# Optimization experiments

Measured on AMD Instinct MI355X. Metric: run time of the kernel, lower is better.

## Reference

```python
import jax, jax.numpy as jnp
import numpy as np

RATIOS = [0.9, 0.7, 0.5, 0.3]
EPS = 1e-5


def _layernorm(x, g, b):
    m = jnp.mean(x, axis=-1, keepdims=True)
    v = jnp.mean(jnp.square(x - m), axis=-1, keepdims=True)
    return (x - m) * jax.lax.rsqrt(v + EPS) * g + b


def _stage(x, g, b, W, bias):
    return _layernorm(x, g, b) @ W + bias


def _prune(x, W1, b1, W2, b2, ratio):
    B, N, C = x.shape
    stats = jnp.mean(x, axis=1)                       # (B, C)
    scores = jax.nn.relu(stats @ W1 + b1) @ W2 + b2    # (B, C)
    k = max(1, int(C * ratio))
    _, idx = jax.lax.top_k(jax.lax.stop_gradient(scores), k)  # (B, k)
    hard = jnp.zeros((B, C), scores.dtype).at[jnp.arange(B)[:, None], idx].set(1.0)
    soft = jax.nn.sigmoid(scores)
    # straight-through: forward value == hard, gradient flows through soft
    mask = hard + soft - jax.lax.stop_gradient(soft)
    return x * mask[:, None, :]


def setup_inputs() -> dict:
    key = jax.random.key(0)
    dims = [(96, 96), (96, 192), (192, 384), (384, 768)]
    inp = {}
    ks = jax.random.split(key, 64)
    ki = iter(ks)
    inp["x"] = jax.random.normal(next(ki), (32, 3136, 96), dtype=jnp.float32)
    for i, (din, dout) in enumerate(dims, 1):
        inp[f"s{i}_g"] = jnp.ones((din,), jnp.float32)
        inp[f"s{i}_b"] = jnp.zeros((din,), jnp.float32)
        inp[f"s{i}_W"] = jax.random.normal(next(ki), (din, dout), jnp.float32) * 0.02
        inp[f"s{i}_bias"] = jnp.zeros((dout,), jnp.float32)
        d = dout
        inp[f"p{i}_W1"] = jax.random.normal(next(ki), (d, d // 4), jnp.float32) * 0.02
        inp[f"p{i}_b1"] = jnp.zeros((d // 4,), jnp.float32)
        inp[f"p{i}_W2"] = jax.random.normal(next(ki), (d // 4, d), jnp.float32) * 0.02
        inp[f"p{i}_b2"] = jnp.zeros((d,), jnp.float32)
    inp["H"] = 56
    inp["W"] = 56
    return inp


def reference(x,
              s1_g, s1_b, s1_W, s1_bias, p1_W1, p1_b1, p1_W2, p1_b2,
              s2_g, s2_b, s2_W, s2_bias, p2_W1, p2_b1, p2_W2, p2_b2,
              s3_g, s3_b, s3_W, s3_bias, p3_W1, p3_b1, p3_W2, p3_b2,
              s4_g, s4_b, s4_W, s4_bias, p4_W1, p4_b1, p4_W2, p4_b2,
              H, W):
    x = _stage(x, s1_g, s1_b, s1_W, s1_bias)
    x = _prune(x, p1_W1, p1_b1, p1_W2, p1_b2, RATIOS[0])
    x = _stage(x, s2_g, s2_b, s2_W, s2_bias)
    x = _prune(x, p2_W1, p2_b1, p2_W2, p2_b2, RATIOS[1])
    x = _stage(x, s3_g, s3_b, s3_W, s3_bias)
    x = _prune(x, p3_W1, p3_b1, p3_W2, p3_b2, RATIOS[2])
    x = _stage(x, s4_g, s4_b, s4_W, s4_bias)
    x = _prune(x, p4_W1, p4_b1, p4_W2, p4_b2, RATIOS[3])
    return x
```

## Files before the change

kernel.cpp:

```cpp
#include <hip/hip_runtime.h>
#include <hip/hip_bf16.h>
#include <stdint.h>

#define NTOK 3136
#define MTOT 100352
#define RPW  14
#define WPB  224

typedef __attribute__((ext_vector_type(8))) short bf16x8;
typedef __attribute__((ext_vector_type(4))) float f32x4;
typedef __attribute__((ext_vector_type(2))) float f32x2;

static __device__ __forceinline__ ushort f2bf(float x) {
  union { float f; uint32_t u; } c; c.f = x;
  uint32_t r = (c.u + 0x7FFFu + ((c.u >> 16) & 1u)) >> 16;
  return (ushort)r;
}
static __device__ __forceinline__ float bf2f(ushort h) {
  union { uint32_t u; float f; } c; c.u = ((uint32_t)h) << 16;
  return c.f;
}

template<int DIN, bool WLO>
__global__ __launch_bounds__(256)
void ln_colsum_k(const float* __restrict__ in, const float* __restrict__ gma,
                 const float* __restrict__ bta, ushort* __restrict__ oh,
                 ushort* __restrict__ ol, float* __restrict__ part)
{
  constexpr int P2 = DIN / 2;
  constexpr int T2 = (P2 + 63) / 64;
  const int wid  = (blockIdx.x * 256 + threadIdx.x) >> 6;
  const int lane = threadIdx.x & 63;
  const int b = wid / WPB;
  const int w = wid - b * WPB;

  f32x2 gv[T2], bv[T2], acc[T2];
#pragma unroll
  for (int t = 0; t < T2; ++t) {
    int c2 = lane + 64 * t;
    if (c2 < P2) {
      gv[t] = *(const f32x2*)(gma + 2 * c2);
      bv[t] = *(const f32x2*)(bta + 2 * c2);
    } else { gv[t] = {0.f, 0.f}; bv[t] = {0.f, 0.f}; }
    acc[t] = {0.f, 0.f};
  }

  const size_t rbase = ((size_t)b * NTOK + (size_t)w * RPW) * DIN;
  const float* ip = in + rbase;
  ushort* oph = oh + rbase;
  ushort* opl = ol + rbase;

  for (int j = 0; j < RPW; ++j) {
    f32x2 v[T2];
    float s = 0.f, sq = 0.f;
#pragma unroll
    for (int t = 0; t < T2; ++t) {
      int c2 = lane + 64 * t;
      f32x2 xv = {0.f, 0.f};
      if (c2 < P2) xv = *(const f32x2*)(ip + (size_t)j * DIN + 2 * c2);
      v[t] = xv;
      s  += xv[0] + xv[1];
      sq += xv[0] * xv[0] + xv[1] * xv[1];
    }
#pragma unroll
    for (int off = 1; off < 64; off <<= 1) {
      s  += __shfl_xor(s, off);
      sq += __shfl_xor(sq, off);
    }
    float m   = s / (float)DIN;
    float var = sq / (float)DIN - m * m;
    float r   = 1.f / sqrtf(var + 1e-5f);
#pragma unroll
    for (int t = 0; t < T2; ++t) {
      int c2 = lane + 64 * t;
      if (c2 < P2) {
        float xn0 = (v[t][0] - m) * r * gv[t][0] + bv[t][0];
        float xn1 = (v[t][1] - m) * r * gv[t][1] + bv[t][1];
        ushort h0 = f2bf(xn0), h1 = f2bf(xn1);
        ((uint32_t*)(oph + (size_t)j * DIN))[c2] =
            (uint32_t)h0 | ((uint32_t)h1 << 16);
        if (WLO) {
          ushort l0 = f2bf(xn0 - bf2f(h0)), l1 = f2bf(xn1 - bf2f(h1));
          ((uint32_t*)(opl + (size_t)j * DIN))[c2] =
              (uint32_t)l0 | ((uint32_t)l1 << 16);
        }
        acc[t][0] += xn0;
        acc[t][1] += xn1;
      }
    }
  }
#pragma unroll
  for (int t = 0; t < T2; ++t) {
    int c2 = lane + 64 * t;
    if (c2 < P2) {
      int c = 2 * c2;
      part[((size_t)b * DIN + c) * WPB + w]     = acc[t][0];
      part[((size_t)b * DIN + c + 1) * WPB + w] = acc[t][1];
    }
  }
}

template<int DIN, int DOUT, int SLOTS, bool CMP, int CMPN, int RLEN, bool GLO>
__global__ __launch_bounds__(1024)
void scores_k(const float* __restrict__ part,
              const float* __restrict__ Wt, const float* __restrict__ bias,
              const float* __restrict__ W1, const float* __restrict__ b1,
              const float* __restrict__ W2, const float* __restrict__ b2,
              float* __restrict__ mask, int k,
              const ushort* __restrict__ whi, const ushort* __restrict__ wlo,
              ushort* __restrict__ wch, ushort* __restrict__ wcl,
              int* __restrict__ list_g, float* __restrict__ biasc)
{
  constexpr int DH  = DOUT / 4;
  constexpr int DH4 = DH / 4;
  constexpr int NSLC = (1024 / DH4 < 64) ? 1024 / DH4 : 64;
  constexpr int RPSC = (DOUT + NSLC - 1) / NSLC;
  constexpr int C4  = DOUT / 4;
  constexpr int NSLD = (1024 / C4 < 64) ? 1024 / C4 : 64;
  constexpr int RPSD = (DH + NSLD - 1) / NSLD;

  __shared__ float xm[DIN];
  __shared__ float st[DOUT];
  __shared__ float h[DH];
  __shared__ float sc[DOUT];
  __shared__ float red[4096];
  __shared__ int lsh[256];

  const int b = blockIdx.x, tid = threadIdx.x;

  if constexpr (SLOTS == 25) {
    if (tid < DIN) {
      const float* p = part + ((size_t)b * DIN + tid) * 25;
      float s = 0.f;
#pragma unroll
      for (int i = 0; i < 25; ++i) s += p[i];
      xm[tid] = s * (1.f / (float)NTOK);
    }
  } else {
    const int cg = tid >> 2, wq = tid & 3;
    if (cg < DIN) {
      const float* p = part + ((size_t)b * DIN + cg) * WPB + wq * 56;
      f32x4 a = {0.f, 0.f, 0.f, 0.f};
#pragma unroll
      for (int u = 0; u < 14; ++u) {
        f32x4 t0 = *(const f32x4*)(p + u * 4);
        a[0] += t0[0]; a[1] += t0[1]; a[2] += t0[2]; a[3] += t0[3];
      }
      red[wq * DIN + cg] = (a[0] + a[1]) + (a[2] + a[3]);
    }
    __syncthreads();
    if (tid < DIN)
      xm[tid] = ((red[0 * DIN + tid] + red[1 * DIN + tid]) +
                 (red[2 * DIN + tid] + red[3 * DIN + tid])) * (1.f / (float)NTOK);
  }
  __syncthreads();

  {
    constexpr int RPS = DIN / 4;
    const int j4 = tid % C4, sl = tid / C4;
    if (sl < 4) {
      const float* wp = Wt + (size_t)(sl * RPS) * DOUT + j4 * 4;
      f32x4 acc = {0.f, 0.f, 0.f, 0.f};
#pragma unroll
      for (int r = 0; r < RPS; ++r) {
        f32x4 wv = *(const f32x4*)(wp + (size_t)r * DOUT);
        float xv = xm[sl * RPS + r];
        acc[0] = fmaf(xv, wv[0], acc[0]);
        acc[1] = fmaf(xv, wv[1], acc[1]);
        acc[2] = fmaf(xv, wv[2], acc[2]);
        acc[3] = fmaf(xv, wv[3], acc[3]);
      }
      *(f32x4*)&red[sl * DOUT + j4 * 4] = acc;
    }
  }
  __syncthreads();
  if (tid < DOUT)
    st[tid] = ((red[0 * DOUT + tid] + red[1 * DOUT + tid]) +
               (red[2 * DOUT + tid] + red[3 * DOUT + tid])) + bias[tid];
  __syncthreads();

  {
    const int j4 = tid % DH4, sl = tid / DH4;
    if (sl < NSLC) {
      f32x4 acc = {0.f, 0.f, 0.f, 0.f};
#pragma unroll
      for (int rr = 0; rr < RPSC; ++rr) {
        int r = sl * RPSC + rr;
        if (r < DOUT) {
          f32x4 wv = *(const f32x4*)(W1 + (size_t)r * DH + j4 * 4);
          float sv = st[r];
          acc[0] = fmaf(sv, wv[0], acc[0]);
          acc[1] = fmaf(sv, wv[1], acc[1]);
          acc[2] = fmaf(sv, wv[2], acc[2]);
          acc[3] = fmaf(sv, wv[3], acc[3]);
        }
      }
      *(f32x4*)&red[(size_t)sl * DH + j4 * 4] = acc;
    }
  }
  __syncthreads();
  if (tid < DH) {
    float a = 0.f;
#pragma unroll 4
    for (int sl = 0; sl < NSLC; ++sl) a += red[(size_t)sl * DH + tid];
    h[tid] = fmaxf(b1[tid] + a, 0.f);
  }
  __syncthreads();

  {
    const int c4 = tid % C4, sl = tid / C4;
    if (sl < NSLD) {
      f32x4 acc = {0.f, 0.f, 0.f, 0.f};
#pragma unroll
      for (int rr = 0; rr < RPSD; ++rr) {
        int r = sl * RPSD + rr;
        if (r < DH) {
          f32x4 wv = *(const f32x4*)(W2 + (size_t)r * DOUT + c4 * 4);
          float hv = h[r];
          acc[0] = fmaf(hv, wv[0], acc[0]);
          acc[1] = fmaf(hv, wv[1], acc[1]);
          acc[2] = fmaf(hv, wv[2], acc[2]);
          acc[3] = fmaf(hv, wv[3], acc[3]);
        }
      }
      *(f32x4*)&red[(size_t)sl * DOUT + c4 * 4] = acc;
    }
  }
  __syncthreads();
  for (int c = tid; c < DOUT; c += 1024) {
    float a = 0.f;
#pragma unroll 4
    for (int sl = 0; sl < NSLD; ++sl) a += red[(size_t)sl * DOUT + c];
    sc[c] = b2[c] + a;
  }
  __syncthreads();

  for (int c = tid; c < DOUT; c += 1024) {
    float v = sc[c];
    int rank = 0;
#pragma unroll 8
    for (int j = 0; j < DOUT; ++j) {
      float u = sc[j];
      rank += (u > v) || (u == v && j < c);
    }
    mask[(size_t)b * DOUT + c] = (rank < k) ? 1.f : 0.f;
    if (CMP && rank < k) lsh[rank] = c;
  }
  if constexpr (CMP) {
    if (tid >= k && tid < CMPN) lsh[tid] = -1;
    __syncthreads();
    if (tid < CMPN) {
      int c = lsh[tid];
      list_g[b * 256 + tid] = c;
      biasc[b * 256 + tid] = (c >= 0) ? bias[c] : 0.f;
    }
    constexpr int U4 = RLEN / 8;
    for (int idx = tid; idx < CMPN * U4; idx += 1024) {
      int j = idx / U4, u = idx - j * U4;
      int src = lsh[j];
      uint4 v = make_uint4(0u, 0u, 0u, 0u);
      if (src >= 0) v = *(const uint4*)(whi + (size_t)src * RLEN + u * 8);
      *(uint4*)(wch + ((size_t)b * CMPN + j) * RLEN + u * 8) = v;
      if constexpr (GLO) {
        uint4 vl = make_uint4(0u, 0u, 0u, 0u);
        if (src >= 0) vl = *(const uint4*)(wlo + (size_t)src * RLEN + u * 8);
        *(uint4*)(wcl + ((size_t)b * CMPN + j) * RLEN + u * 8) = vl;
      }
    }
  }
}

__global__ __launch_bounds__(256)
void convW_all_k(const float* __restrict__ W0, const float* __restrict__ W1,
                 const float* __restrict__ W2, const float* __restrict__ W3,
                 ushort* __restrict__ hi, ushort* __restrict__ lo)
{
  const int Kd[4]   = { 96, 96, 192, 384 };
  const int Nd[4]   = { 96, 192, 384, 768 };
  const int off[5]  = { 0, 12288, 36864, 110592, 405504 };
  const float* Wp[4] = { W0, W1, W2, W3 };

  int idx = blockIdx.x * 256 + threadIdx.x;
  if (idx >= 405504) return;
  int s = (idx >= off[1]) + (idx >= off[2]) + (idx >= off[3]);
  int local = idx - off[s];
  int K = Kd[s], N = Nd[s];
  int n = local / K, kk = local - n * K;
  float v = (n < N) ? Wp[s][(size_t)kk * N + n] : 0.f;
  ushort h = f2bf(v);
  hi[idx] = h;
  lo[idx] = f2bf(v - bf2f(h));
}

#define ASYNC16(GP, LP) __builtin_amdgcn_global_load_lds( \
    (const __attribute__((address_space(1))) void*)(GP),  \
    (__attribute__((address_space(3))) void*)(LP), 16, 0, 0)

template<int K, int BNL, int N, int NWN, bool WLO>
__global__ __launch_bounds__(128 * NWN)
void gemm_ln_k(const ushort* __restrict__ ahi, const ushort* __restrict__ alo,
               const ushort* __restrict__ bhi, const ushort* __restrict__ blo,
               const float* __restrict__ bias, const float* __restrict__ msk,
               const float* __restrict__ gnext, const float* __restrict__ bnext,
               ushort* __restrict__ oh, ushort* __restrict__ ol,
               float* __restrict__ part)
{
  constexpr int T   = 128 * NWN;
  constexpr int R   = T / 4;
  constexpr int AI  = 128 / R;
  constexpr int BI  = BNL / R;
  constexpr int KS  = K / 32;
  constexpr int WN  = N / NWN;
  constexpr int NFR = WN / 16;
  __shared__ __align__(16) ushort ldsAh[2][128 * 32];
  __shared__ __align__(16) ushort ldsAl[2][128 * 32];
  __shared__ __align__(16) ushort ldsBh[2][BNL * 32];
  __shared__ __align__(16) ushort ldsBl[2][BNL * 32];

  const int tid  = threadIdx.x;
  const int lane = tid & 63;
  const int wid  = tid >> 6;
  const int wm = wid & 1, wn = wid >> 1;

  const int q8  = gridDim.x >> 3;
  const int bid = blockIdx.x;
  const int mt  = (bid & 7) * q8 + (bid >> 3);
  const size_t row0 = (size_t)mt * 128;

  f32x4 acc[4][NFR];
#pragma unroll
  for (int i = 0; i < 4; ++i)
#pragma unroll
    for (int j = 0; j < NFR; ++j) acc[i][j] = { 0.f, 0.f, 0.f, 0.f };

  const int c_row  = tid >> 2;
  const int c_phys = tid & 3;

#define STG(BUF, KK)                                                           \
  {                                                                            \
    const int k0_ = (KK) * 32;                                                 \
    _Pragma("unroll")                                                          \
    for (int r_ = 0; r_ < AI; ++r_) {                                          \
      int row_  = c_row + r_ * R;                                              \
      int slot_ = c_phys ^ ((row_ >> 1) & 3);                                  \
      ASYNC16(ahi + (row0 + row_) * (size_t)K + (k0_ + slot_ * 8),             \
              &ldsAh[BUF][(row_ * 4 + c_phys) * 8]);                           \
      ASYNC16(alo + (row0 + row_) * (size_t)K + (k0_ + slot_ * 8),             \
              &ldsAl[BUF][(row_ * 4 + c_phys) * 8]);                           \
    }                                                                          \
    _Pragma("unroll")                                                          \
    for (int r_ = 0; r_ < BI; ++r_) {                                          \
      int row_  = c_row + r_ * R;                                              \
      int slot_ = c_phys ^ ((row_ >> 1) & 3);                                  \
      ASYNC16(bhi + (size_t)row_ * K + (k0_ + slot_ * 8),                      \
              &ldsBh[BUF][(row_ * 4 + c_phys) * 8]);                           \
      ASYNC16(blo + (size_t)row_ * K + (k0_ + slot_ * 8),                      \
              &ldsBl[BUF][(row_ * 4 + c_phys) * 8]);                           \
    }                                                                          \
  }

  STG(0, 0);
  asm volatile("s_waitcnt vmcnt(0)" ::: "memory");
  __builtin_amdgcn_s_barrier();
#pragma unroll
  for (int t = 0; t < KS; ++t) {
    if (t + 1 < KS) STG((t + 1) & 1, t + 1);
    const int buf = t & 1;
    const int slot = lane >> 4;
    const int r16  = lane & 15;
    bf16x8 ah[4], al[4], bh[NFR], bl[NFR];
#pragma unroll
    for (int mi = 0; mi < 4; ++mi) {
      int r = wm * 64 + mi * 16 + r16;
      int off = (r * 4 + (slot ^ ((r >> 1) & 3))) * 8;
      ah[mi] = *(const bf16x8*)&ldsAh[buf][off];
      al[mi] = *(const bf16x8*)&ldsAl[buf][off];
    }
#pragma unroll
    for (int ni = 0; ni < NFR; ++ni) {
      int r = wn * WN + ni * 16 + r16;
      int off = (r * 4 + (slot ^ ((r >> 1) & 3))) * 8;
      bh[ni] = *(const bf16x8*)&ldsBh[buf][off];
      bl[ni] = *(const bf16x8*)&ldsBl[buf][off];
    }
#pragma unroll
    for (int mi = 0; mi < 4; ++mi)
#pragma unroll
      for (int ni = 0; ni < NFR; ++ni)
        acc[mi][ni] = __builtin_amdgcn_mfma_f32_16x16x32_bf16(ah[mi], bh[ni],
                                                              acc[mi][ni], 0, 0, 0);
#pragma unroll
    for (int mi = 0; mi < 4; ++mi)
#pragma unroll
      for (int ni = 0; ni < NFR; ++ni)
        acc[mi][ni] = __builtin_amdgcn_mfma_f32_16x16x32_bf16(ah[mi], bl[ni],
                                                              acc[mi][ni], 0, 0, 0);
#pragma unroll
    for (int mi = 0; mi < 4; ++mi)
#pragma unroll
      for (int ni = 0; ni < NFR; ++ni)
        acc[mi][ni] = __builtin_amdgcn_mfma_f32_16x16x32_bf16(al[mi], bh[ni],
                                                              acc[mi][ni], 0, 0, 0);
    if (t + 1 < KS) {
      asm volatile("s_waitcnt vmcnt(0)" ::: "memory");
      __builtin_amdgcn_s_barrier();
    }
  }
#undef STG

  __syncthreads();

  float* rowred = (float*)&ldsAh[0][0];
  float* colred = (float*)&ldsAl[0][0];
  ushort* xsh = (ushort*)&ldsBh[0][0];
  ushort* xsl = (ushort*)&ldsBl[0][0];

  const int l15 = lane & 15, l4 = lane >> 4;
  const int b0i = (int)(row0 / NTOK);
  const size_t rowB = (size_t)(b0i + 1) * NTOK;
  const bool strad = rowB < row0 + 128;

  float biasv[NFR], mk0a[NFR], mk1a[NFR], gvn[NFR], bvn[NFR];
#pragma unroll
  for (int ni = 0; ni < NFR; ++ni) {
    int n = wn * WN + ni * 16 + l15;
    biasv[ni] = bias[n];
    mk0a[ni] = msk[(size_t)b0i * N + n];
    mk1a[ni] = strad ? msk[(size_t)(b0i + 1) * N + n] : mk0a[ni];
    gvn[ni] = gnext[n];
    bvn[ni] = bnext[n];
  }

  float rs[16], rq[16];
#pragma unroll
  for (int i = 0; i < 16; ++i) { rs[i] = 0.f; rq[i] = 0.f; }
#pragma unroll
  for (int mi = 0; mi < 4; ++mi)
#pragma unroll
    for (int q = 0; q < 4; ++q) {
      size_t row = row0 + wm * 64 + mi * 16 + l4 * 4 + q;
      bool loB = row < rowB;
#pragma unroll
      for (int ni = 0; ni < NFR; ++ni) {
        float v = (acc[mi][ni][q] + biasv[ni]) * (loB ? mk0a[ni] : mk1a[ni]);
        acc[mi][ni][q] = v;
        rs[mi * 4 + q] += v;
        rq[mi * 4 + q] += v * v;
      }
    }
#pragma unroll
  for (int off = 1; off < 16; off <<= 1)
#pragma unroll
    for (int i = 0; i < 16; ++i) {
      rs[i] += __shfl_xor(rs[i], off);
      rq[i] += __shfl_xor(rq[i], off);
    }
  if (l15 == 0) {
#pragma unroll
    for (int mi = 0; mi < 4; ++mi)
#pragma unroll
      for (int q = 0; q < 4; ++q) {
        int r = wm * 64 + mi * 16 + l4 * 4 + q;
        rowred[(wn * 128 + r) * 2 + 0] = rs[mi * 4 + q];
        rowred[(wn * 128 + r) * 2 + 1] = rq[mi * 4 + q];
      }
  }
  __syncthreads();

  float mean[16], rstd[16];
#pragma unroll
  for (int mi = 0; mi < 4; ++mi)
#pragma unroll
    for (int q = 0; q < 4; ++q) {
      int r = wm * 64 + mi * 16 + l4 * 4 + q;
      float S = 0.f, Q = 0.f;
#pragma unroll
      for (int w = 0; w < NWN; ++w) {
        S += rowred[(w * 128 + r) * 2 + 0];
        Q += rowred[(w * 128 + r) * 2 + 1];
      }
      float mn  = S / (float)N;
      float var = Q / (float)N - mn * mn;
      mean[mi * 4 + q] = mn;
      rstd[mi * 4 + q] = 1.f / sqrtf(var + 1e-5f);
    }

  float cs0[NFR], cs1[NFR];
#pragma unroll
  for (int ni = 0; ni < NFR; ++ni) { cs0[ni] = 0.f; cs1[ni] = 0.f; }
#pragma unroll
  for (int mi = 0; mi < 4; ++mi) {
    __syncthreads();
#pragma unroll
    for (int q = 0; q < 4; ++q) {
      const int rl = l4 * 4 + q;
      const size_t row = row0 + wm * 64 + mi * 16 + rl;
      const bool loB = row < rowB;
      const float mn = mean[mi * 4 + q], rv = rstd[mi * 4 + q];
#pragma unroll
      for (int ni = 0; ni < NFR; ++ni) {
        const int n = wn * WN + ni * 16 + l15;
        float xn = (acc[mi][ni][q] - mn) * rv * gvn[ni] + bvn[ni];
        ushort hh = f2bf(xn);
        xsh[(wm * 16 + rl) * N + n] = hh;
        if constexpr (WLO) xsl[(wm * 16 + rl) * N + n] = f2bf(xn - bf2f(hh));
        if (loB) cs0[ni] += xn; else cs1[ni] += xn;
      }
    }
    __syncthreads();
    constexpr int U4R = N / 8;
    for (int idx = tid; idx < 32 * U4R; idx += T) {
      const int grp = idx / U4R, c = idx - grp * U4R;
      const size_t row = row0 + (grp >> 4) * 64 + mi * 16 + (grp & 15);
      *(uint4*)(oh + row * (size_t)N + c * 8) =
          *(const uint4*)(xsh + grp * N + c * 8);
      if constexpr (WLO)
        *(uint4*)(ol + row * (size_t)N + c * 8) =
            *(const uint4*)(xsl + grp * N + c * 8);
    }
  }

#pragma unroll
  for (int ni = 0; ni < NFR; ++ni) {
    cs0[ni] += __shfl_xor(cs0[ni], 16);
    cs0[ni] += __shfl_xor(cs0[ni], 32);
    cs1[ni] += __shfl_xor(cs1[ni], 16);
    cs1[ni] += __shfl_xor(cs1[ni], 32);
  }
  __syncthreads();
  if (l4 == 0) {
#pragma unroll
    for (int ni = 0; ni < NFR; ++ni) {
      int n = wn * WN + ni * 16 + l15;
      colred[(0 * 2 + wm) * N + n] = cs0[ni];
      colred[(1 * 2 + wm) * N + n] = cs1[ni];
    }
  }
  __syncthreads();
  if (wm == 0 && l4 == 0) {
    const int mt_lo = (b0i * NTOK) >> 7;
    const int slot0 = mt - mt_lo;
#pragma unroll
    for (int ni = 0; ni < NFR; ++ni) {
      int n = wn * WN + ni * 16 + l15;
      float t0 = colred[0 * N + n] + colred[1 * N + n];
      part[((size_t)b0i * N + n) * 25 + slot0] = t0;
      if (strad) {
        float t1 = colred[2 * N + n] + colred[3 * N + n];
        part[((size_t)(b0i + 1) * N + n) * 25 + 0] = t1;
      }
    }
  }
}

template<int K, int NC, int N>
__global__ __launch_bounds__(256)
void gemm_lnc_k(const ushort* __restrict__ ahi, const ushort* __restrict__ alo,
                const ushort* __restrict__ wch, const ushort* __restrict__ wcl,
                const int* __restrict__ list, const float* __restrict__ biasc,
                const float* __restrict__ gnext, const float* __restrict__ bnext,
                ushort* __restrict__ oh, float* __restrict__ part)
{
  constexpr int KS  = K / 32;
  constexpr int WN  = NC / 2;
  constexpr int NFR = WN / 16;
  __shared__ __align__(16) ushort ldsAh[2][128 * 32];
  __shared__ __align__(16) ushort ldsAl[2][128 * 32];
  __shared__ __align__(16) ushort ldsBh[2][NC * 32];
  __shared__ __align__(16) ushort ldsBl[2][NC * 32];

  const int tid  = threadIdx.x;
  const int lane = tid & 63;
  const int wid  = tid >> 6;
  const int wm = wid & 1, wn = wid >> 1;

  const int q8  = gridDim.x >> 3;
  const int bid = blockIdx.x;
  const int wg  = (bid & 7) * q8 + (bid >> 3);
  const int b   = wg / 25;
  const int mt  = wg - b * 25;
  const size_t row0 = (size_t)b * NTOK + (size_t)mt * 128;
  const size_t rowEnd = (size_t)(b + 1) * NTOK;
  const int rows_valid = (mt == 24) ? 64 : 128;

  const ushort* bph = wch + (size_t)b * NC * K;
  const ushort* bpl = wcl + (size_t)b * NC * K;

  f32x4 acc[4][NFR];
#pragma unroll
  for (int i = 0; i < 4; ++i)
#pragma unroll
    for (int j = 0; j < NFR; ++j) acc[i][j] = { 0.f, 0.f, 0.f, 0.f };

  const int c_row  = tid >> 2;
  const int c_phys = tid & 3;

#define STGL(BUF, KK)                                                          \
  {                                                                            \
    const int k0_ = (KK) * 32;                                                 \
    _Pragma("unroll")                                                          \
    for (int r_ = 0; r_ < 2; ++r_) {                                           \
      int row_  = c_row + r_ * 64;                                             \
      int slot_ = c_phys ^ ((row_ >> 1) & 3);                                  \
      size_t ar_ = row0 + row_;                                                \
      if (ar_ >= rowEnd) ar_ = rowEnd - 1;                                     \
      ASYNC16(ahi + ar_ * (size_t)K + (k0_ + slot_ * 8),                       \
              &ldsAh[BUF][(row_ * 4 + c_phys) * 8]);                           \
      ASYNC16(alo + ar_ * (size_t)K + (k0_ + slot_ * 8),                       \
              &ldsAl[BUF][(row_ * 4 + c_phys) * 8]);                           \
    }                                                                          \
    _Pragma("unroll")                                                          \
    for (int r_ = 0; r_ < 3; ++r_) {                                           \
      int row_  = c_row + r_ * 64;                                             \
      int slot_ = c_phys ^ ((row_ >> 1) & 3);                                  \
      ASYNC16(bph + (size_t)row_ * K + (k0_ + slot_ * 8),                      \
              &ldsBh[BUF][(row_ * 4 + c_phys) * 8]);                           \
      ASYNC16(bpl + (size_t)row_ * K + (k0_ + slot_ * 8),                      \
              &ldsBl[BUF][(row_ * 4 + c_phys) * 8]);                           \
    }                                                                          \
  }

  STGL(0, 0);
  asm volatile("s_waitcnt vmcnt(0)" ::: "memory");
  __builtin_amdgcn_s_barrier();
#pragma unroll
  for (int t = 0; t < KS; ++t) {
    if (t + 1 < KS) STGL((t + 1) & 1, t + 1);
    const int buf = t & 1;
    const int slot = lane >> 4;
    const int r16  = lane & 15;
    bf16x8 ah[4], al[4], bh[NFR], bl[NFR];
#pragma unroll
    for (int mi = 0; mi < 4; ++mi) {
      int r = wm * 64 + mi * 16 + r16;
      int off = (r * 4 + (slot ^ ((r >> 1) & 3))) * 8;
      ah[mi] = *(const bf16x8*)&ldsAh[buf][off];
      al[mi] = *(const bf16x8*)&ldsAl[buf][off];
    }
#pragma unroll
    for (int ni = 0; ni < NFR; ++ni) {
      int r = wn * WN + ni * 16 + r16;
      int off = (r * 4 + (slot ^ ((r >> 1) & 3))) * 8;
      bh[ni] = *(const bf16x8*)&ldsBh[buf][off];
      bl[ni] = *(const bf16x8*)&ldsBl[buf][off];
    }
#pragma unroll
    for (int mi = 0; mi < 4; ++mi)
#pragma unroll
      for (int ni = 0; ni < NFR; ++ni)
        acc[mi][ni] = __builtin_amdgcn_mfma_f32_16x16x32_bf16(ah[mi], bh[ni],
                                                              acc[mi][ni], 0, 0, 0);
#pragma unroll
    for (int mi = 0; mi < 4; ++mi)
#pragma unroll
      for (int ni = 0; ni < NFR; ++ni)
        acc[mi][ni] = __builtin_amdgcn_mfma_f32_16x16x32_bf16(ah[mi], bl[ni],
                                                              acc[mi][ni], 0, 0, 0);
#pragma unroll
    for (int mi = 0; mi < 4; ++mi)
#pragma unroll
      for (int ni = 0; ni < NFR; ++ni)
        acc[mi][ni] = __builtin_amdgcn_mfma_f32_16x16x32_bf16(al[mi], bh[ni],
                                                              acc[mi][ni], 0, 0, 0);
    if (t + 1 < KS) {
      asm volatile("s_waitcnt vmcnt(0)" ::: "memory");
      __builtin_amdgcn_s_barrier();
    }
  }
#undef STGL

  __syncthreads();

  float* rr      = (float*)&ldsAh[0][0];
  float* rowredp = rr;
  float* rowmnrv = rr + 512;
  float* rowrv   = rr + 640;
  float* sbuf    = (float*)&ldsBh[0][0];

  const int l15 = lane & 15, l4 = lane >> 4;

  int   nj[NFR];
  float biasv[NFR];
#pragma unroll
  for (int ni = 0; ni < NFR; ++ni) {
    int j = wn * WN + ni * 16 + l15;
    nj[ni]    = list[b * 256 + j];
    biasv[ni] = biasc[b * 256 + j];
  }

  float rs[16], rq[16];
#pragma unroll
  for (int i = 0; i < 16; ++i) { rs[i] = 0.f; rq[i] = 0.f; }
#pragma unroll
  for (int mi = 0; mi < 4; ++mi)
#pragma unroll
    for (int q = 0; q < 4; ++q) {
#pragma unroll
      for (int ni = 0; ni < NFR; ++ni) {
        float v = acc[mi][ni][q] + biasv[ni];
        acc[mi][ni][q] = v;
        rs[mi * 4 + q] += v;
        rq[mi * 4 + q] += v * v;
      }
    }
#pragma unroll
  for (int off = 1; off < 16; off <<= 1)
#pragma unroll
    for (int i = 0; i < 16; ++i) {
      rs[i] += __shfl_xor(rs[i], off);
      rq[i] += __shfl_xor(rq[i], off);
    }
  if (l15 == 0) {
#pragma unroll
    for (int mi = 0; mi < 4; ++mi)
#pragma unroll
      for (int q = 0; q < 4; ++q) {
        int r = wm * 64 + mi * 16 + l4 * 4 + q;
        rowredp[(wn * 128 + r) * 2 + 0] = rs[mi * 4 + q];
        rowredp[(wn * 128 + r) * 2 + 1] = rq[mi * 4 + q];
      }
  }
  __syncthreads();
  if (tid < 128) {
    float S = rowredp[(0 * 128 + tid) * 2 + 0] + rowredp[(1 * 128 + tid) * 2 + 0];
    float Q = rowredp[(0 * 128 + tid) * 2 + 1] + rowredp[(1 * 128 + tid) * 2 + 1];
    float mn = S / (float)N;
    float rv = 1.f / sqrtf(Q / (float)N - mn * mn + 1e-5f);
    rowmnrv[tid] = mn * rv;
    rowrv[tid]   = rv;
  }
  __syncthreads();

  float colS = 0.f, colS2 = 0.f;

#pragma unroll
  for (int h = 0; h < 8; ++h) {
    if (h * 16 >= rows_valid) break;
    __syncthreads();
    for (int idx = tid; idx < 16 * N / 4; idx += 256)
      ((f32x4*)sbuf)[idx] = f32x4{0.f, 0.f, 0.f, 0.f};
    __syncthreads();
    if ((h >> 2) == wm) {
      const int mi = h & 3;
#pragma unroll
      for (int q = 0; q < 4; ++q) {
        const int rl = l4 * 4 + q;
        const float rv = rowrv[h * 16 + rl];
#pragma unroll
        for (int ni = 0; ni < NFR; ++ni)
          sbuf[rl * N + nj[ni]] = acc[mi][ni][q] * rv;
      }
    }
    __syncthreads();
    {
      float a = 0.f;
#pragma unroll
      for (int rl = 0; rl < 16; ++rl) a += sbuf[rl * N + tid];
      colS += a;
      if (tid < N - 256) {
        float a2 = 0.f;
        const int c2 = 256 + tid;
#pragma unroll
        for (int rl = 0; rl < 16; ++rl) a2 += sbuf[rl * N + c2];
        colS2 += a2;
      }
    }
    for (int idx = tid; idx < 16 * (N / 8); idx += 256) {
      const int rl = idx / (N / 8), cg = idx - rl * (N / 8);
      const float mnrv = rowmnrv[h * 16 + rl];
      const float* sp = sbuf + rl * N + cg * 8;
      f32x4 s0 = *(const f32x4*)(sp);
      f32x4 s1 = *(const f32x4*)(sp + 4);
      f32x4 g0 = *(const f32x4*)(gnext + cg * 8);
      f32x4 g1 = *(const f32x4*)(gnext + cg * 8 + 4);
      f32x4 e0 = *(const f32x4*)(bnext + cg * 8);
      f32x4 e1 = *(const f32x4*)(bnext + cg * 8 + 4);
      uint32_t w[4];
#pragma unroll
      for (int j = 0; j < 2; ++j) {
        ushort ha = f2bf(g0[2*j]   * (s0[2*j]   - mnrv) + e0[2*j]);
        ushort hb = f2bf(g0[2*j+1] * (s0[2*j+1] - mnrv) + e0[2*j+1]);
        w[j] = (uint32_t)ha | ((uint32_t)hb << 16);
      }
#pragma unroll
      for (int j = 0; j < 2; ++j) {
        ushort ha = f2bf(g1[2*j]   * (s1[2*j]   - mnrv) + e1[2*j]);
        ushort hb = f2bf(g1[2*j+1] * (s1[2*j+1] - mnrv) + e1[2*j+1]);
        w[2 + j] = (uint32_t)ha | ((uint32_t)hb << 16);
      }
      *(uint4*)(oh + (row0 + h * 16 + rl) * (size_t)N + cg * 8) =
          make_uint4(w[0], w[1], w[2], w[3]);
    }
  }

  float msum = 0.f;
  for (int r = 0; r < rows_valid; ++r) msum += rowmnrv[r];
  {
    const int c = tid;
    part[((size_t)b * N + c) * 25 + mt] =
        gnext[c] * (colS - msum) + (float)rows_valid * bnext[c];
    if (tid < N - 256) {
      const int c2 = 256 + tid;
      part[((size_t)b * N + c2) * 25 + mt] =
          gnext[c2] * (colS2 - msum) + (float)rows_valid * bnext[c2];
    }
  }
}

template<int K>
__global__ __launch_bounds__(512)
void gemm_c4_k(const ushort* __restrict__ A, const ushort* __restrict__ Wc,
               const int* __restrict__ list, const float* __restrict__ biasc,
               float* __restrict__ C)
{
  constexpr int NT = K / 32;
  __shared__ __align__(16) ushort ldsA[3][128 * 32];
  __shared__ __align__(16) ushort ldsB[3][256 * 32];

  const int tid  = threadIdx.x;
  const int lane = tid & 63;
  const int wid  = tid >> 6;
  const int wm = wid & 1, wn = wid >> 1;

  const int q8  = gridDim.x >> 3;
  const int bid = blockIdx.x;
  const int wg  = (bid & 7) * q8 + (bid >> 3);
  const int b   = wg / 25;
  const int mt  = wg - b * 25;
  const size_t row0 = (size_t)b * NTOK + (size_t)mt * 128;
  const int rows_valid = (mt == 24) ? 64 : 128;

  const ushort* bp = Wc + (size_t)b * 256 * K;

  const int c_row  = tid >> 2;
  const int c_phys = tid & 3;

  size_t arow = row0 + c_row;
  const size_t rowEnd = (size_t)(b + 1) * NTOK;
  if (arow >= rowEnd) arow = rowEnd - 1;
  const ushort* apr = A + arow * (size_t)K;

  f32x4 acc[4][4];
#pragma unroll
  for (int i = 0; i < 4; ++i)
#pragma unroll
    for (int j = 0; j < 4; ++j) acc[i][j] = { 0.f, 0.f, 0.f, 0.f };

#define STAGEC(BUF, TT)                                                        \
  {                                                                            \
    const int k0_ = (TT) * 32;                                                 \
    {                                                                          \
      int slot_ = c_phys ^ ((c_row >> 1) & 3);                                 \
      ASYNC16(apr + (k0_ + slot_ * 8),                                         \
              &ldsA[BUF][(c_row * 4 + c_phys) * 8]);                           \
    }                                                                          \
    _Pragma("unroll")                                                          \
    for (int r_ = 0; r_ < 2; ++r_) {                                           \
      int row_  = c_row + r_ * 128;                                            \
      int slot_ = c_phys ^ ((row_ >> 1) & 3);                                  \
      ASYNC16(bp + (size_t)row_ * K + (k0_ + slot_ * 8),                       \
              &ldsB[BUF][(row_ * 4 + c_phys) * 8]);                            \
    }                                                                          \
  }

  STAGEC(0, 0);
  STAGEC(1, 1);
#pragma unroll
  for (int t = 0; t < NT; ++t) {
    if (t == NT - 1) { asm volatile("s_waitcnt vmcnt(0)" ::: "memory"); }
    else             { asm volatile("s_waitcnt vmcnt(3)" ::: "memory"); }
    __builtin_amdgcn_s_barrier();
    if (t + 2 < NT) STAGEC((t + 2) % 3, t + 2);
    const int buf = t % 3;
    const int slot = lane >> 4;
    const int r16  = lane & 15;
    bf16x8 af[4], bfr[4];
#pragma unroll
    for (int mi = 0; mi < 4; ++mi) {
      int r = wm * 64 + mi * 16 + r16;
      af[mi] = *(const bf16x8*)&ldsA[buf][(r * 4 + (slot ^ ((r >> 1) & 3))) * 8];
    }
#pragma unroll
    for (int ni = 0; ni < 4; ++ni) {
      int r = wn * 64 + ni * 16 + r16;
      bfr[ni] = *(const bf16x8*)&ldsB[buf][(r * 4 + (slot ^ ((r >> 1) & 3))) * 8];
    }
#pragma unroll
    for (int mi = 0; mi < 4; ++mi)
#pragma unroll
      for (int ni = 0; ni < 4; ++ni)
        acc[mi][ni] = __builtin_amdgcn_mfma_f32_16x16x32_bf16(af[mi], bfr[ni],
                                                              acc[mi][ni], 0, 0, 0);
  }
#undef STAGEC

  float* cst = (float*)&ldsB[0][0];

  const int l15 = lane & 15, l4 = lane >> 4;
  int   nj[4];
  float biasv[4];
#pragma unroll
  for (int ni = 0; ni < 4; ++ni) {
    int j = wn * 64 + ni * 16 + l15;
    nj[ni]    = list[b * 256 + j];
    biasv[ni] = biasc[b * 256 + j];
  }

#pragma unroll
  for (int hh = 0; hh < 8; ++hh) {
    const int hrows = rows_valid - hh * 16;
    if (hrows <= 0) break;
    __syncthreads();
    for (int idx = tid; idx < 16 * 192; idx += 512)
      ((f32x4*)cst)[idx] = f32x4{0.f, 0.f, 0.f, 0.f};
    __syncthreads();
    if ((hh >> 2) == wm) {
      const int mi = hh & 3;
#pragma unroll
      for (int q = 0; q < 4; ++q) {
        const int rl = l4 * 4 + q;
#pragma unroll
        for (int ni = 0; ni < 4; ++ni)
          if (nj[ni] >= 0)
            cst[rl * 768 + nj[ni]] = acc[mi][ni][q] + biasv[ni];
      }
    }
    __syncthreads();
    const int nst = (hrows >= 16 ? 16 : hrows) * 192;
    for (int idx = tid; idx < nst; idx += 512) {
      const int grp = idx / 192, c = idx - grp * 192;
      const size_t row = row0 + hh * 16 + grp;
      *(f32x4*)(C + row * 768 + c * 4) = ((const f32x4*)cst)[grp * 192 + c];
    }
  }
}

extern "C" void kernel_launch(void* const* d_in, const int* in_sizes, int n_in,
                              void* d_out, int out_size, void* d_ws, size_t ws_size,
                              hipStream_t stream)
{
  (void)in_sizes; (void)n_in; (void)out_size; (void)ws_size;
  const float* x = (const float*)d_in[0];
  const float *sg[4], *sb[4], *sW[4], *sbias[4], *pW1[4], *pb1[4], *pW2[4], *pb2[4];
  for (int s = 0; s < 4; ++s) {
    int base = 1 + s * 8;
    sg[s]    = (const float*)d_in[base + 0];
    sb[s]    = (const float*)d_in[base + 1];
    sW[s]    = (const float*)d_in[base + 2];
    sbias[s] = (const float*)d_in[base + 3];
    pW1[s]   = (const float*)d_in[base + 4];
    pb1[s]   = (const float*)d_in[base + 5];
    pW2[s]   = (const float*)d_in[base + 6];
    pb2[s]   = (const float*)d_in[base + 7];
  }

  float* out = (float*)d_out;
  ushort* hiA = (ushort*)out;
  ushort* loA = (ushort*)(out + 19267584);
  ushort* loB = (ushort*)(out + 38535168);

  char* ws = (char*)d_ws;
  ushort* hiB  = (ushort*)(ws);
  float*  part = (float*) (ws + 77070336);
  float*  mk   = (float*) (ws + 79822848);
  ushort* w_hi = (ushort*)(ws + 79921152);
  ushort* w_lo = (ushort*)(ws + 80732160);
  ushort* wc   = (ushort*)(ws + 81543168);
  int*    lst  = (int*)   (ws + 87834624);
  float*  bsc  = (float*) (ws + 87867392);

  ushort* wch3 = wc;
  ushort* wcl3 = wc + 1179648;

  const int woff[4] = { 0, 12288, 36864, 110592 };

  convW_all_k<<<(405504 + 255) / 256, 256, 0, stream>>>(
      sW[0], sW[1], sW[2], sW[3], w_hi, w_lo);

  const int LNG = 32 * WPB / 4;

  ln_colsum_k<96, true><<<LNG, 256, 0, stream>>>(x, sg[0], sb[0], hiA, loA, part);
  scores_k<96, 96, 224, false, 256, 384, false><<<32, 1024, 0, stream>>>(
      part, sW[0], sbias[0], pW1[0], pb1[0], pW2[0], pb2[0], mk, 86,
      nullptr, nullptr, nullptr, nullptr, nullptr, nullptr);
  gemm_ln_k<96, 128, 96, 2, true><<<784, 256, 0, stream>>>(
      hiA, loA, w_hi + woff[0], w_lo + woff[0],
      sbias[0], mk, sg[1], sb[1], hiB, loB, part);

  scores_k<96, 192, 25, false, 256, 384, false><<<32, 1024, 0, stream>>>(
      part, sW[1], sbias[1], pW1[1], pb1[1], pW2[1], pb2[1], mk, 134,
      nullptr, nullptr, nullptr, nullptr, nullptr, nullptr);
  gemm_ln_k<96, 192, 192, 2, true><<<784, 256, 0, stream>>>(
      hiB, loB, w_hi + woff[1], w_lo + woff[1],
      sbias[1], mk, sg[2], sb[2], hiA, loA, part);

  scores_k<192, 384, 25, true, 192, 192, true><<<32, 1024, 0, stream>>>(
      part, sW[2], sbias[2], pW1[2], pb1[2], pW2[2], pb2[2], mk, 192,
      w_hi + woff[2], w_lo + woff[2], wch3, wcl3, lst, bsc);
  gemm_lnc_k<192, 192, 384><<<800, 256, 0, stream>>>(
      hiA, loA, wch3, wcl3, lst, bsc, sg[3], sb[3], hiB, part);

  scores_k<384, 768, 25, true, 256, 384, false><<<32, 1024, 0, stream>>>(
      part, sW[3], sbias[3], pW1[3], pb1[3], pW2[3], pb2[3], mk, 230,
      w_hi + woff[3], nullptr, wc, nullptr, lst, bsc);
  gemm_c4_k<384><<<800, 512, 0, stream>>>(hiB, wc, lst, bsc, out);
}
```

Measured before the change: 461.9 us.

## Gather selected weight rows directly in GEMMs and single-buffer gemm_ln LDS

Drops the per-batch compaction of selected weight rows in scores_k. The compacted GEMMs now load B rows straight from the full converted weight arrays through per-thread row indices taken from the selection list, which removes a global write plus reread of the compacted weights. gemm_ln_k also moves from double-buffered LDS staging to a single buffer, with a full wait and barrier each K step. That halves its shared memory and may raise occupancy, but it stops overlapping loads with MFMA work.

Measured after the change: 452.9 us. About the same (-2.0%).

```diff
diff --git a/kernel.cpp b/kernel.cpp
--- a/kernel.cpp
+++ b/kernel.cpp
@@ -100,15 +100,13 @@
   }
 }
 
-template<int DIN, int DOUT, int SLOTS, bool CMP, int CMPN, int RLEN, bool GLO>
+template<int DIN, int DOUT, int SLOTS, bool CMP, int CMPN>
 __global__ __launch_bounds__(1024)
 void scores_k(const float* __restrict__ part,
               const float* __restrict__ Wt, const float* __restrict__ bias,
               const float* __restrict__ W1, const float* __restrict__ b1,
               const float* __restrict__ W2, const float* __restrict__ b2,
               float* __restrict__ mask, int k,
-              const ushort* __restrict__ whi, const ushort* __restrict__ wlo,
-              ushort* __restrict__ wch, ushort* __restrict__ wcl,
               int* __restrict__ list_g, float* __restrict__ biasc)
 {
   constexpr int DH  = DOUT / 4;
@@ -253,19 +251,6 @@
       int c = lsh[tid];
       list_g[b * 256 + tid] = c;
       biasc[b * 256 + tid] = (c >= 0) ? bias[c] : 0.f;
-    }
-    constexpr int U4 = RLEN / 8;
-    for (int idx = tid; idx < CMPN * U4; idx += 1024) {
-      int j = idx / U4, u = idx - j * U4;
-      int src = lsh[j];
-      uint4 v = make_uint4(0u, 0u, 0u, 0u);
-      if (src >= 0) v = *(const uint4*)(whi + (size_t)src * RLEN + u * 8);
-      *(uint4*)(wch + ((size_t)b * CMPN + j) * RLEN + u * 8) = v;
-      if constexpr (GLO) {
-        uint4 vl = make_uint4(0u, 0u, 0u, 0u);
-        if (src >= 0) vl = *(const uint4*)(wlo + (size_t)src * RLEN + u * 8);
-        *(uint4*)(wcl + ((size_t)b * CMPN + j) * RLEN + u * 8) = vl;
-      }
     }
   }
 }
@@ -312,10 +297,10 @@
   constexpr int KS  = K / 32;
   constexpr int WN  = N / NWN;
   constexpr int NFR = WN / 16;
-  __shared__ __align__(16) ushort ldsAh[2][128 * 32];
-  __shared__ __align__(16) ushort ldsAl[2][128 * 32];
-  __shared__ __align__(16) ushort ldsBh[2][BNL * 32];
-  __shared__ __align__(16) ushort ldsBl[2][BNL * 32];
+  __shared__ __align__(16) ushort ldsAh[128 * 32];
+  __shared__ __align__(16) ushort ldsAl[128 * 32];
+  __shared__ __align__(16) ushort ldsBh[BNL * 32];
+  __shared__ __align__(16) ushort ldsBl[BNL * 32];
 
   const int tid  = threadIdx.x;
   const int lane = tid & 63;
@@ -336,7 +321,7 @@
   const int c_row  = tid >> 2;
   const int c_phys = tid & 3;
 
-#define STG(BUF, KK)                                                           \
+#define STG(KK)                                                                \
   {                                                                            \
     const int k0_ = (KK) * 32;                                                 \
     _Pragma("unroll")                                                          \
@@ -344,28 +329,26 @@
       int row_  = c_row + r_ * R;                                              \
       int slot_ = c_phys ^ ((row_ >> 1) & 3);                                  \
       ASYNC16(ahi + (row0 + row_) * (size_t)K + (k0_ + slot_ * 8),             \
-              &ldsAh[BUF][(row_ * 4 + c_phys) * 8]);                           \
+              &ldsAh[(row_ * 4 + c_phys) * 8]);                                \
       ASYNC16(alo + (row0 + row_) * (size_t)K + (k0_ + slot_ * 8),             \
-              &ldsAl[BUF][(row_ * 4 + c_phys) * 8]);                           \
+              &ldsAl[(row_ * 4 + c_phys) * 8]);                                \
     }                                                                          \
     _Pragma("unroll")                                                          \
     for (int r_ = 0; r_ < BI; ++r_) {                                          \
       int row_  = c_row + r_ * R;                                              \
       int slot_ = c_phys ^ ((row_ >> 1) & 3);                                  \
       ASYNC16(bhi + (size_t)row_ * K + (k0_ + slot_ * 8),                      \
-              &ldsBh[BUF][(row_ * 4 + c_phys) * 8]);                           \
+              &ldsBh[(row_ * 4 + c_phys) * 8]);                                \
       ASYNC16(blo + (size_t)row_ * K + (k0_ + slot_ * 8),                      \
-              &ldsBl[BUF][(row_ * 4 + c_phys) * 8]);                           \
+              &ldsBl[(row_ * 4 + c_phys) * 8]);                                \
     }                                                                          \
   }
 
-  STG(0, 0);
-  asm volatile("s_waitcnt vmcnt(0)" ::: "memory");
-  __builtin_amdgcn_s_barrier();
 #pragma unroll
   for (int t = 0; t < KS; ++t) {
-    if (t + 1 < KS) STG((t + 1) & 1, t + 1);
-    const int buf = t & 1;
+    STG(t);
+    asm volatile("s_waitcnt vmcnt(0)" ::: "memory");
+    __builtin_amdgcn_s_barrier();
     const int slot = lane >> 4;
     const int r16  = lane & 15;
     bf16x8 ah[4], al[4], bh[NFR], bl[NFR];
@@ -373,15 +356,15 @@
     for (int mi = 0; mi < 4; ++mi) {
       int r = wm * 64 + mi * 16 + r16;
       int off = (r * 4 + (slot ^ ((r >> 1) & 3))) * 8;
-      ah[mi] = *(const bf16x8*)&ldsAh[buf][off];
-      al[mi] = *(const bf16x8*)&ldsAl[buf][off];
+      ah[mi] = *(const bf16x8*)&ldsAh[off];
+      al[mi] = *(const bf16x8*)&ldsAl[off];
     }
 #pragma unroll
     for (int ni = 0; ni < NFR; ++ni) {
       int r = wn * WN + ni * 16 + r16;
       int off = (r * 4 + (slot ^ ((r >> 1) & 3))) * 8;
-      bh[ni] = *(const bf16x8*)&ldsBh[buf][off];
-      bl[ni] = *(const bf16x8*)&ldsBl[buf][off];
+      bh[ni] = *(const bf16x8*)&ldsBh[off];
+      bl[ni] = *(const bf16x8*)&ldsBl[off];
     }
 #pragma unroll
     for (int mi = 0; mi < 4; ++mi)
@@ -401,19 +384,16 @@
       for (int ni = 0; ni < NFR; ++ni)
         acc[mi][ni] = __builtin_amdgcn_mfma_f32_16x16x32_bf16(al[mi], bh[ni],
                                                               acc[mi][ni], 0, 0, 0);
-    if (t + 1 < KS) {
-      asm volatile("s_waitcnt vmcnt(0)" ::: "memory");
-      __builtin_amdgcn_s_barrier();
-    }
+    if (t + 1 < KS) __builtin_amdgcn_s_barrier();
   }
 #undef STG
 
   __syncthreads();
 
-  float* rowred = (float*)&ldsAh[0][0];
-  float* colred = (float*)&ldsAl[0][0];
-  ushort* xsh = (ushort*)&ldsBh[0][0];
-  ushort* xsl = (ushort*)&ldsBl[0][0];
+  float* rowred = (float*)&ldsAh[0];
+  float* colred = (float*)&ldsAl[0];
+  ushort* xsh = (ushort*)&ldsBh[0];
+  ushort* xsl = (ushort*)&ldsBl[0];
 
   const int l15 = lane & 15, l4 = lane >> 4;
   const int b0i = (int)(row0 / NTOK);
@@ -556,7 +536,7 @@
 template<int K, int NC, int N>
 __global__ __launch_bounds__(256)
 void gemm_lnc_k(const ushort* __restrict__ ahi, const ushort* __restrict__ alo,
-                const ushort* __restrict__ wch, const ushort* __restrict__ wcl,
+                const ushort* __restrict__ whi, const ushort* __restrict__ wlo,
                 const int* __restrict__ list, const float* __restrict__ biasc,
                 const float* __restrict__ gnext, const float* __restrict__ bnext,
                 ushort* __restrict__ oh, float* __restrict__ part)
@@ -583,17 +563,21 @@
   const size_t rowEnd = (size_t)(b + 1) * NTOK;
   const int rows_valid = (mt == 24) ? 64 : 128;
 
-  const ushort* bph = wch + (size_t)b * NC * K;
-  const ushort* bpl = wcl + (size_t)b * NC * K;
-
-  f32x4 acc[4][NFR];
-#pragma unroll
-  for (int i = 0; i < 4; ++i)
-#pragma unroll
-    for (int j = 0; j < NFR; ++j) acc[i][j] = { 0.f, 0.f, 0.f, 0.f };
-
   const int c_row  = tid >> 2;
   const int c_phys = tid & 3;
+
+  int bsrc[3];
+#pragma unroll
+  for (int r_ = 0; r_ < 3; ++r_) {
+    int s = list[b * 256 + c_row + r_ * 64];
+    bsrc[r_] = (s < 0) ? 0 : s;
+  }
+
+  f32x4 acc[4][NFR];
+#pragma unroll
+  for (int i = 0; i < 4; ++i)
+#pragma unroll
+    for (int j = 0; j < NFR; ++j) acc[i][j] = { 0.f, 0.f, 0.f, 0.f };
 
 #define STGL(BUF, KK)                                                          \
   {                                                                            \
@@ -613,9 +597,9 @@
     for (int r_ = 0; r_ < 3; ++r_) {                                           \
       int row_  = c_row + r_ * 64;                                             \
       int slot_ = c_phys ^ ((row_ >> 1) & 3);                                  \
-      ASYNC16(bph + (size_t)row_ * K + (k0_ + slot_ * 8),                      \
+      ASYNC16(whi + (size_t)bsrc[r_] * K + (k0_ + slot_ * 8),                  \
               &ldsBh[BUF][(row_ * 4 + c_phys) * 8]);                           \
-      ASYNC16(bpl + (size_t)row_ * K + (k0_ + slot_ * 8),                      \
+      ASYNC16(wlo + (size_t)bsrc[r_] * K + (k0_ + slot_ * 8),                  \
               &ldsBl[BUF][(row_ * 4 + c_phys) * 8]);                           \
     }                                                                          \
   }
@@ -809,7 +793,7 @@
 
 template<int K>
 __global__ __launch_bounds__(512)
-void gemm_c4_k(const ushort* __restrict__ A, const ushort* __restrict__ Wc,
+void gemm_c4_k(const ushort* __restrict__ A, const ushort* __restrict__ whi,
                const int* __restrict__ list, const float* __restrict__ biasc,
                float* __restrict__ C)
 {
@@ -830,8 +814,6 @@
   const size_t row0 = (size_t)b * NTOK + (size_t)mt * 128;
   const int rows_valid = (mt == 24) ? 64 : 128;
 
-  const ushort* bp = Wc + (size_t)b * 256 * K;
-
   const int c_row  = tid >> 2;
   const int c_phys = tid & 3;
 
@@ -839,6 +821,13 @@
   const size_t rowEnd = (size_t)(b + 1) * NTOK;
   if (arow >= rowEnd) arow = rowEnd - 1;
   const ushort* apr = A + arow * (size_t)K;
+
+  int bsrc[2];
+#pragma unroll
+  for (int r_ = 0; r_ < 2; ++r_) {
+    int s = list[b * 256 + c_row + r_ * 128];
+    bsrc[r_] = (s < 0) ? 0 : s;
+  }
 
   f32x4 acc[4][4];
 #pragma unroll
@@ -858,7 +847,7 @@
     for (int r_ = 0; r_ < 2; ++r_) {                                           \
       int row_  = c_row + r_ * 128;                                            \
       int slot_ = c_phys ^ ((row_ >> 1) & 3);                                  \
-      ASYNC16(bp + (size_t)row_ * K + (k0_ + slot_ * 8),                       \
+      ASYNC16(whi + (size_t)bsrc[r_] * K + (k0_ + slot_ * 8),                  \
               &ldsB[BUF][(row_ * 4 + c_phys) * 8]);                            \
     }                                                                          \
   }
@@ -965,13 +954,9 @@
   float*  mk   = (float*) (ws + 79822848);
   ushort* w_hi = (ushort*)(ws + 79921152);
   ushort* w_lo = (ushort*)(ws + 80732160);
-  ushort* wc   = (ushort*)(ws + 81543168);
   int*    lst  = (int*)   (ws + 87834624);
   float*  bsc  = (float*) (ws + 87867392);
 
-  ushort* wch3 = wc;
-  ushort* wcl3 = wc + 1179648;
-
   const int woff[4] = { 0, 12288, 36864, 110592 };
 
   convW_all_k<<<(405504 + 255) / 256, 256, 0, stream>>>(
@@ -980,28 +965,29 @@
   const int LNG = 32 * WPB / 4;
 
   ln_colsum_k<96, true><<<LNG, 256, 0, stream>>>(x, sg[0], sb[0], hiA, loA, part);
-  scores_k<96, 96, 224, false, 256, 384, false><<<32, 1024, 0, stream>>>(
+  scores_k<96, 96, 224, false, 256><<<32, 1024, 0, stream>>>(
       part, sW[0], sbias[0], pW1[0], pb1[0], pW2[0], pb2[0], mk, 86,
-      nullptr, nullptr, nullptr, nullptr, nullptr, nullptr);
+      nullptr, nullptr);
   gemm_ln_k<96, 128, 96, 2, true><<<784, 256, 0, stream>>>(
       hiA, loA, w_hi + woff[0], w_lo + woff[0],
       sbias[0], mk, sg[1], sb[1], hiB, loB, part);
 
-  scores_k<96, 192, 25, false, 256, 384, false><<<32, 1024, 0, stream>>>(
+  scores_k<96, 192, 25, false, 256><<<32, 1024, 0, stream>>>(
       part, sW[1], sbias[1], pW1[1], pb1[1], pW2[1], pb2[1], mk, 134,
-      nullptr, nullptr, nullptr, nullptr, nullptr, nullptr);
+      nullptr, nullptr);
   gemm_ln_k<96, 192, 192, 2, true><<<784, 256, 0, stream>>>(
       hiB, loB, w_hi + woff[1], w_lo + woff[1],
       sbias[1], mk, sg[2], sb[2], hiA, loA, part);
 
-  scores_k<192, 384, 25, true, 192, 192, true><<<32, 1024, 0, stream>>>(
+  scores_k<192, 384, 25, true, 192><<<32, 1024, 0, stream>>>(
       part, sW[2], sbias[2], pW1[2], pb1[2], pW2[2], pb2[2], mk, 192,
-      w_hi + woff[2], w_lo + woff[2], wch3, wcl3, lst, bsc);
+      lst, bsc);
   gemm_lnc_k<192, 192, 384><<<800, 256, 0, stream>>>(
-      hiA, loA, wch3, wcl3, lst, bsc, sg[3], sb[3], hiB, part);
-
-  scores_k<384, 768, 25, true, 256, 384, false><<<32, 1024, 0, stream>>>(
+      hiA, loA, w_hi + woff[2], w_lo + woff[2], lst, bsc, sg[3], sb[3],
+      hiB, part);
+
+  scores_k<384, 768, 25, true, 256><<<32, 1024, 0, stream>>>(
       part, sW[3], sbias[3], pW1[3], pb1[3], pW2[3], pb2[3], mk, 230,
-      w_hi + woff[3], nullptr, wc, nullptr, lst, bsc);
-  gemm_c4_k<384><<<800, 512, 0, stream>>>(hiB, wc, lst, bsc, out);
+      lst, bsc);
+  gemm_c4_k<384><<<800, 512, 0, stream>>>(hiB, w_hi + woff[3], lst, bsc, out);
 }
```
